# Performance work log

Measured on AMD Instinct MI355X. Metric: run time of the kernel, lower is better.

The kernel has to match this reference:

```python
import jax, jax.numpy as jnp
import numpy as np

N_NODES = 100000
N_EDGES = 1280000
IN_DIM = 64
HID = 64
OUT_DIM = 2
N_GRAPHS = 1000
BN_EPS = 1e-5


def setup_inputs() -> dict:
    key = jax.random.key(0)
    ks = jax.random.split(key, 16)
    x = jax.random.normal(ks[0], (N_NODES, IN_DIM), dtype=jnp.float32)
    edge_index = jax.random.randint(ks[1], (2, N_EDGES), 0, N_NODES, dtype=jnp.int64)
    batch = jnp.sort(jax.random.randint(ks[2], (N_NODES,), 0, N_GRAPHS, dtype=jnp.int64))
    # He-init linear weights (stored as [in, out] so forward is x @ W)
    def he(k, fan_in, fan_out):
        return jax.random.normal(k, (fan_in, fan_out), dtype=jnp.float32) * np.sqrt(2.0 / fan_in)
    return {
        "x": x,
        "edge_index": edge_index,
        "batch": batch,
        "bn_in_g": jnp.ones((IN_DIM,), jnp.float32),
        "bn_in_b": jnp.zeros((IN_DIM,), jnp.float32),
        "W1": he(ks[3], IN_DIM, HID), "b1": jnp.zeros((HID,), jnp.float32),
        "g1": jnp.ones((HID,), jnp.float32), "be1": jnp.zeros((HID,), jnp.float32),
        "W2": he(ks[4], HID, HID), "b2": jnp.zeros((HID,), jnp.float32),
        "g2": jnp.ones((HID,), jnp.float32), "be2": jnp.zeros((HID,), jnp.float32),
        "Wout": he(ks[5], HID, OUT_DIM), "bout": jnp.zeros((OUT_DIM,), jnp.float32),
    }


def _batchnorm(x, g, b):
    # training-mode BN over the node dimension (biased variance, as torch uses for normalization)
    m = jnp.mean(x, axis=0)
    v = jnp.mean(jnp.square(x - m), axis=0)
    return (x - m) * jax.lax.rsqrt(v + BN_EPS) * g + b


def _gcn_norm(edge_index, n):
    # PyG GCNConv normalization with added self-loops:
    # norm_e = deg[src]^-1/2 * deg[dst]^-1/2, deg computed on A + I over targets.
    row = jnp.concatenate([edge_index[0], jnp.arange(n, dtype=edge_index.dtype)])
    col = jnp.concatenate([edge_index[1], jnp.arange(n, dtype=edge_index.dtype)])
    deg = jax.ops.segment_sum(jnp.ones_like(col, dtype=jnp.float32), col, num_segments=n)
    dinv = jnp.where(deg > 0, jax.lax.rsqrt(deg), 0.0)
    norm = dinv[row] * dinv[col]
    return row, col, norm


def _gcn_conv(x, W, b, row, col, norm, n):
    h = x @ W                                   # [N, out]
    msg = h[row] * norm[:, None]                # gather over edges (incl. self-loops)
    agg = jax.ops.segment_sum(msg, col, num_segments=n)
    return agg + b


def reference(x, edge_index, batch, bn_in_g, bn_in_b, W1, b1, g1, be1, W2, b2, g2, be2, Wout, bout):
    n = x.shape[0]
    row, col, norm = _gcn_norm(edge_index, n)
    h = _batchnorm(x, bn_in_g, bn_in_b)         # input BN (dropout = identity in eval)
    h = _gcn_conv(h, W1, b1, row, col, norm, n)
    h = _batchnorm(jax.nn.relu(h), g1, be1)
    h = _gcn_conv(h, W2, b2, row, col, norm, n)
    h = _batchnorm(jax.nn.relu(h), g2, be2)
    # global mean pool per graph
    sums = jax.ops.segment_sum(h, batch, num_segments=N_GRAPHS)
    cnts = jax.ops.segment_sum(jnp.ones((n,), h.dtype), batch, num_segments=N_GRAPHS)
    pooled = sums / jnp.maximum(cnts, 1.0)[:, None]
    return pooled @ Wout + bout                 # [N_GRAPHS, OUT_DIM]
```

## Files before the change

### kernel.cpp

```cpp
#include <hip/hip_runtime.h>
#include <math.h>

#define N_NODES 100000
#define N_EDGES 1280000
#define DIM 64
#define N_GRAPHS 1000
#define BN_EPS 1e-5f
#define NB 392
#define P1B 256
#define P1E 5000
#define SB 400
#define WIN 64
#define NWIN (N_EDGES / WIN)
#define NSLOT 32

__device__ __forceinline__ unsigned int bf16_rtn2(float a, float b) {
    unsigned int ua = __float_as_uint(a);
    unsigned int ub = __float_as_uint(b);
    ua = (ua + 0x7FFFu + ((ua >> 16) & 1u)) >> 16;
    ub = (ub + 0x7FFFu + ((ub >> 16) & 1u)) >> 16;
    return ua | (ub << 16);
}
__device__ __forceinline__ unsigned short bf16r(float a) {
    unsigned int u = __float_as_uint(a);
    return (unsigned short)((u + 0x7FFFu + ((u >> 16) & 1u)) >> 16);
}
__device__ __forceinline__ float bfup(unsigned short u) {
    return __uint_as_float(((unsigned int)u) << 16);
}
__device__ __forceinline__ float blo(unsigned int v) { return __uint_as_float(v << 16); }
__device__ __forceinline__ float bhi(unsigned int v) { return __uint_as_float(v & 0xFFFF0000u); }

__global__ __launch_bounds__(256) void k_p1hist(const int* __restrict__ ei,
                                                const int* __restrict__ batch,
                                                const float* __restrict__ X,
                                                int* __restrict__ bh,
                                                int* __restrict__ start,
                                                float* __restrict__ gsum,
                                                float* __restrict__ gsumsq) {
    int t = threadIdx.x;
    if (blockIdx.x < P1B) {
        __shared__ int hist[NB];
        for (int b = t; b < NB; b += 256) hist[b] = 0;
        __syncthreads();
        int e0 = blockIdx.x * P1E;
        #pragma unroll 4
        for (int e = e0 + t; e < e0 + P1E; e += 256)
            atomicAdd(&hist[ei[N_EDGES + e] >> 8], 1);
        __syncthreads();
        for (int b = t; b < NB; b += 256) bh[b * P1B + blockIdx.x] = hist[b];
    } else if (blockIdx.x < P1B + SB) {
        int grp = blockIdx.x - P1B;
        int j = t & 63, rg = t >> 6;
        int base = grp * 250;
        float s = 0.f, s2 = 0.f;
        for (int i = base + rg; i < base + 250; i += 4) {
            float v = X[i * DIM + j];
            s += v; s2 += v * v;
        }
        __shared__ float ls[256], ls2[256];
        ls[t] = s; ls2[t] = s2;
        __syncthreads();
        if (t < 64) {
            int slot = (grp & (NSLOT - 1)) * DIM;
            s  = ls[j]  + ls[64 + j]  + ls[128 + j]  + ls[192 + j];
            s2 = ls2[j] + ls2[64 + j] + ls2[128 + j] + ls2[192 + j];
            atomicAdd(&gsum[slot + j], s);
            atomicAdd(&gsumsq[slot + j], s2);
        }
    } else {
        int i = (blockIdx.x - P1B - SB) * 256 + t;
        if (i < N_NODES) {
            int cur = batch[i];
            if (i == 0) { for (int q = 0; q <= cur; q++) start[q] = 0; }
            else {
                int prev = batch[i - 1];
                for (int q = prev + 1; q <= cur; q++) start[q] = i;
            }
            if (i == N_NODES - 1)
                for (int q = cur + 1; q <= N_GRAPHS; q++) start[q] = N_NODES;
        }
    }
}

__global__ void k_scan1(const int* __restrict__ bh, int* __restrict__ iscan,
                        int* __restrict__ bsum) {
    __shared__ int ls[256];
    int i = blockIdx.x * 256 + threadIdx.x;
    int v = bh[i];
    ls[threadIdx.x] = v;
    __syncthreads();
    for (int off = 1; off < 256; off <<= 1) {
        int tv = (threadIdx.x >= off) ? ls[threadIdx.x - off] : 0;
        __syncthreads();
        ls[threadIdx.x] += tv;
        __syncthreads();
    }
    iscan[i] = ls[threadIdx.x];
    if (threadIdx.x == 255) bsum[blockIdx.x] = ls[255];
}

__global__ void k_scan2(const int* __restrict__ bsum, int* __restrict__ boff) {
    __shared__ int ls[512];
    int t = threadIdx.x;
    int v0 = (t < NB) ? bsum[t] : 0;
    ls[t] = v0;
    __syncthreads();
    for (int off = 1; off < 512; off <<= 1) {
        int v = (t >= off) ? ls[t - off] : 0;
        __syncthreads();
        ls[t] += v;
        __syncthreads();
    }
    if (t < NB) boff[t] = ls[t] - v0;
}

__global__ __launch_bounds__(256) void k_p1scat(const int* __restrict__ ei,
                                                const int* __restrict__ bh,
                                                const int* __restrict__ iscan,
                                                const int* __restrict__ boff,
                                                int* __restrict__ tmp) {
    __shared__ int cur[NB];
    int blk = blockIdx.x;
    for (int b = threadIdx.x; b < NB; b += 256) {
        int i = b * P1B + blk;
        cur[b] = boff[b] + iscan[i] - bh[i];
    }
    __syncthreads();
    int e0 = blk * P1E;
    for (int e = e0 + threadIdx.x; e < e0 + P1E; e += 256) {
        int r = ei[e], c = ei[N_EDGES + e];
        int pos = atomicAdd(&cur[c >> 8], 1);
        tmp[pos] = (r << 8) | (c & 255);
    }
}

__global__ __launch_bounds__(256) void k_p2a(const int* __restrict__ tmp,
                                             const int* __restrict__ bh,
                                             const int* __restrict__ iscan,
                                             const int* __restrict__ boff,
                                             int* __restrict__ rowstart,
                                             float* __restrict__ dinv,
                                             int* __restrict__ winnode,
                                             float* __restrict__ C) {
    int b = blockIdx.x, t = threadIdx.x;
    int bstart = boff[b] + iscan[b * 256] - bh[b * 256];
    int bend = (b == NB - 1) ? N_EDGES
                             : (boff[b + 1] + iscan[(b + 1) * 256] - bh[(b + 1) * 256]);
    __shared__ int cnt[256], scn[256];
    cnt[t] = 0;
    __syncthreads();
    for (int e = bstart + t; e < bend; e += 256)
        atomicAdd(&cnt[tmp[e] & 255], 1);
    __syncthreads();
    scn[t] = cnt[t];
    __syncthreads();
    for (int off = 1; off < 256; off <<= 1) {
        int v = (t >= off) ? scn[t - off] : 0;
        __syncthreads();
        scn[t] += v;
        __syncthreads();
    }
    int node = b * 256 + t;
    int deg = cnt[t];
    int rs = bstart + scn[t] - deg;
    bool span = false;
    if (node <= N_NODES) rowstart[node] = rs;
    if (node == N_NODES) rowstart[node + 1] = rs;
    if (node < N_NODES) {
        dinv[node] = 1.0f / sqrtf((float)(deg + 1));
        int re = rs + deg;
        for (int w = (rs + WIN - 1) / WIN; w * WIN < re; ++w) winnode[w] = node;
        span = (deg > 0) && (rs / WIN != (re - 1) / WIN);
    }
    int lane = t & 63;
    int wbase = b * 256 + (t & ~63);
    unsigned long long m = __ballot(span);
    while (m) {
        int bit = __builtin_ctzll(m);
        m &= m - 1;
        C[(size_t)(wbase + bit) * DIM + lane] = 0.f;
    }
}

__global__ __launch_bounds__(256) void k_p2b(const int* __restrict__ tmp,
                                             const int* __restrict__ bh,
                                             const int* __restrict__ iscan,
                                             const int* __restrict__ boff,
                                             const int* __restrict__ rowstart,
                                             int* __restrict__ csr) {
    int b = blockIdx.x, t = threadIdx.x;
    int bstart = boff[b] + iscan[b * 256] - bh[b * 256];
    int bend = (b == NB - 1) ? N_EDGES
                             : (boff[b + 1] + iscan[(b + 1) * 256] - bh[(b + 1) * 256]);
    __shared__ int curs[256];
    int node = b * 256 + t;
    curs[t] = (node < N_NODES) ? rowstart[node] : 0;
    __syncthreads();
    for (int e = bstart + t; e < bend; e += 256) {
        int rec = tmp[e];
        int pos = atomicAdd(&curs[rec & 255], 1);
        csr[pos] = (int)((unsigned)rec >> 8);
    }
}

__global__ void k_bnfold(float* __restrict__ gsum, float* __restrict__ gsumsq,
                         const float* __restrict__ g, const float* __restrict__ b,
                         const float* __restrict__ W,
                         float* __restrict__ scale, float* __restrict__ cshift) {
    int j = threadIdx.x;
    float ms = 0.f, m2 = 0.f;
    for (int k = 0; k < NSLOT; k++) {
        ms += gsum[k * DIM + j];   gsum[k * DIM + j] = 0.f;
        m2 += gsumsq[k * DIM + j]; gsumsq[k * DIM + j] = 0.f;
    }
    float mean = ms * (1.0f / N_NODES);
    float var  = m2 * (1.0f / N_NODES) - mean * mean;
    float inv  = 1.0f / sqrtf(var + BN_EPS);
    float sc   = g[j] * inv;
    scale[j] = sc;
    __shared__ float shl[64];
    shl[j] = b[j] - mean * sc;
    __syncthreads();
    float s = 0.f;
    for (int k = 0; k < DIM; k++) s += shl[k] * W[k * DIM + j];
    cshift[j] = s;
}

__global__ void k_bnfinal(const float* __restrict__ gsum, const float* __restrict__ gsumsq,
                          const float* __restrict__ g, const float* __restrict__ b,
                          float* __restrict__ scale, float* __restrict__ shift) {
    int j = threadIdx.x;
    float ms = 0.f, m2 = 0.f;
    for (int k = 0; k < NSLOT; k++) { ms += gsum[k * DIM + j]; m2 += gsumsq[k * DIM + j]; }
    float mean = ms * (1.0f / N_NODES);
    float var  = m2 * (1.0f / N_NODES) - mean * mean;
    float inv  = 1.0f / sqrtf(var + BN_EPS);
    float sc   = g[j] * inv;
    scale[j] = sc;
    shift[j] = b[j] - mean * sc;
}

__global__ __launch_bounds__(256) void k_gemm_f32(const float* __restrict__ X,
                                                  const float* __restrict__ W,
                                                  const float* __restrict__ scale,
                                                  const float* __restrict__ cshift,
                                                  const float* __restrict__ dinv,
                                                  unsigned short* __restrict__ T) {
    __shared__ float Wl[64 * 64];
    __shared__ float Al[64 * 65];
    for (int t = threadIdx.x; t < 4096; t += 256) Wl[t] = W[t] * scale[t >> 6];
    int row0 = blockIdx.x * 64;
    for (int t = threadIdx.x; t < 4096; t += 256) {
        int r = t >> 6, k = t & 63;
        int i = row0 + r;
        Al[r * 65 + k] = (i < N_NODES) ? X[(size_t)i * DIM + k] : 0.f;
    }
    __syncthreads();
    int r = threadIdx.x & 63;
    int q = threadIdx.x >> 6;
    float acc[16];
    #pragma unroll
    for (int jj = 0; jj < 16; jj++) acc[jj] = cshift[q * 16 + jj];
    #pragma unroll 4
    for (int k = 0; k < 64; k++) {
        float a = Al[r * 65 + k];
        const float4* wv = (const float4*)&Wl[k * 64 + q * 16];
        float4 w0 = wv[0], w1 = wv[1], w2 = wv[2], w3 = wv[3];
        acc[0]  += a * w0.x; acc[1]  += a * w0.y; acc[2]  += a * w0.z; acc[3]  += a * w0.w;
        acc[4]  += a * w1.x; acc[5]  += a * w1.y; acc[6]  += a * w1.z; acc[7]  += a * w1.w;
        acc[8]  += a * w2.x; acc[9]  += a * w2.y; acc[10] += a * w2.z; acc[11] += a * w2.w;
        acc[12] += a * w3.x; acc[13] += a * w3.y; acc[14] += a * w3.z; acc[15] += a * w3.w;
    }
    int i = row0 + r;
    if (i < N_NODES) {
        float dv = dinv[i];
        unsigned int pk[8];
        #pragma unroll
        for (int jj = 0; jj < 8; jj++)
            pk[jj] = bf16_rtn2(acc[2 * jj] * dv, acc[2 * jj + 1] * dv);
        uint4* outv = (uint4*)&T[(size_t)i * DIM + q * 16];
        outv[0] = make_uint4(pk[0], pk[1], pk[2], pk[3]);
        outv[1] = make_uint4(pk[4], pk[5], pk[6], pk[7]);
    }
}

__global__ __launch_bounds__(256) void k_gemm_b16(const unsigned short* __restrict__ X,
                                                  const float* __restrict__ W,
                                                  const float* __restrict__ scale,
                                                  const float* __restrict__ cshift,
                                                  const float* __restrict__ dinv,
                                                  unsigned short* __restrict__ T) {
    __shared__ float Wl[64 * 64];
    __shared__ float Al[64 * 65];
    for (int t = threadIdx.x; t < 4096; t += 256) Wl[t] = W[t] * scale[t >> 6];
    int row0 = blockIdx.x * 64;
    for (int t = threadIdx.x; t < 4096; t += 256) {
        int r = t >> 6, k = t & 63;
        int i = row0 + r;
        Al[r * 65 + k] = (i < N_NODES) ? bfup(X[(size_t)i * DIM + k]) : 0.f;
    }
    __syncthreads();
    int r = threadIdx.x & 63;
    int q = threadIdx.x >> 6;
    float acc[16];
    #pragma unroll
    for (int jj = 0; jj < 16; jj++) acc[jj] = cshift[q * 16 + jj];
    #pragma unroll 4
    for (int k = 0; k < 64; k++) {
        float a = Al[r * 65 + k];
        const float4* wv = (const float4*)&Wl[k * 64 + q * 16];
        float4 w0 = wv[0], w1 = wv[1], w2 = wv[2], w3 = wv[3];
        acc[0]  += a * w0.x; acc[1]  += a * w0.y; acc[2]  += a * w0.z; acc[3]  += a * w0.w;
        acc[4]  += a * w1.x; acc[5]  += a * w1.y; acc[6]  += a * w1.z; acc[7]  += a * w1.w;
        acc[8]  += a * w2.x; acc[9]  += a * w2.y; acc[10] += a * w2.z; acc[11] += a * w2.w;
        acc[12] += a * w3.x; acc[13] += a * w3.y; acc[14] += a * w3.z; acc[15] += a * w3.w;
    }
    int i = row0 + r;
    if (i < N_NODES) {
        float dv = dinv[i];
        unsigned int pk[8];
        #pragma unroll
        for (int jj = 0; jj < 8; jj++)
            pk[jj] = bf16_rtn2(acc[2 * jj] * dv, acc[2 * jj + 1] * dv);
        uint4* outv = (uint4*)&T[(size_t)i * DIM + q * 16];
        outv[0] = make_uint4(pk[0], pk[1], pk[2], pk[3]);
        outv[1] = make_uint4(pk[4], pk[5], pk[6], pk[7]);
    }
}


#define SWZ(S) __builtin_amdgcn_ds_swizzle(csrv, (((S) << 5) | 0x10))

#define ISSUE(SRCV, TVV, B) do {                                      \
    SRCV[0] = SWZ(4 * (B) + 0); SRCV[1] = SWZ(4 * (B) + 1);           \
    SRCV[2] = SWZ(4 * (B) + 2); SRCV[3] = SWZ(4 * (B) + 3);           \
    TVV[0] = T2[(unsigned)SRCV[0] * 16u + cc];                        \
    TVV[1] = T2[(unsigned)SRCV[1] * 16u + cc];                        \
    TVV[2] = T2[(unsigned)SRCV[2] * 16u + cc];                        \
    TVV[3] = T2[(unsigned)SRCV[3] * 16u + cc];                        \
} while (0)

#define STEP(TVV, U, B, FL) do {                                      \
    const int ebs = e0 + 16 * (B) + 4 * (U);                          \
    uint2 tvv = TVV[U];                                               \
    float a0 = blo(tvv.x), a1 = bhi(tvv.x);                           \
    float a2 = blo(tvv.y), a3 = bhi(tvv.y);                           \
    if (re > ebs + 3) {                                               \
        acc0 += a0; acc1 += a1; acc2 += a2; acc3 += a3;               \
    } else {                                                          \
        int lo = ebs;                                                 \
        while (re <= ebs + 3) {                                       \
            int eg = ebs + gg;                                        \
            if (eg >= lo && eg < re) {                                \
                acc0 += a0; acc1 += a1; acc2 += a2; acc3 += a3;       \
            }                                                         \
            lo = re;                                                  \
            FL();                                                     \
        }                                                             \
        if (ebs + gg >= lo) {                                         \
            acc0 += a0; acc1 += a1; acc2 += a2; acc3 += a3;           \
        }                                                             \
    }                                                                 \
} while (0)

#define CONSUME(TVV, B, FL) do {                                      \
    STEP(TVV, 0, B, FL); STEP(TVV, 1, B, FL);                         \
    STEP(TVV, 2, B, FL); STEP(TVV, 3, B, FL);                         \
} while (0)

#define COMB4()                                                       \
    float t0 = acc0 + __shfl_xor(acc0, 16); t0 += __shfl_xor(t0, 32); \
    float t1 = acc1 + __shfl_xor(acc1, 16); t1 += __shfl_xor(t1, 32); \
    float t2 = acc2 + __shfl_xor(acc2, 16); t2 += __shfl_xor(t2, 32); \
    float t3 = acc3 + __shfl_xor(acc3, 16); t3 += __shfl_xor(t3, 32);

#define ADVANCE() do {                                                \
    acc0 = acc1 = acc2 = acc3 = 0.f;                                  \
    ++i; ++k;                                                         \
    if (k < 64) re = __builtin_amdgcn_readlane(rsv, k);               \
    else        re = __builtin_amdgcn_readfirstlane(rowstart[i + 1]); \
    tsv = T2[(unsigned)i * 16u + cc];                                 \
} while (0)

#define FLUSH1() do {                                                 \
    COMB4();                                                          \
    if (part) {                                                       \
        if (lane < 16) {                                              \
            float* cp = &C[(size_t)i * DIM + 4 * cc];                 \
            atomicAdd(cp + 0, t0); atomicAdd(cp + 1, t1);             \
            atomicAdd(cp + 2, t2); atomicAdd(cp + 3, t3);             \
        }                                                             \
        part = false;                                                 \
    } else {                                                          \
        int cnt = i - i0;                                             \
        float di;                                                     \
        if (cnt < 64)                                                 \
            di = __int_as_float(                                      \
                __builtin_amdgcn_readlane(__float_as_int(dv), cnt));  \
        else di = dinv[i];                                            \
        float h0 = fmaxf((t0 + blo(tsv.x)) * di + bb.x, 0.f);         \
        float h1 = fmaxf((t1 + bhi(tsv.x)) * di + bb.y, 0.f);         \
        float h2 = fmaxf((t2 + blo(tsv.y)) * di + bb.z, 0.f);         \
        float h3 = fmaxf((t3 + bhi(tsv.y)) * di + bb.w, 0.f);         \
        if (lane < 16)                                                \
            ((uint2*)H)[(unsigned)i * 16u + cc] =                     \
                make_uint2(bf16_rtn2(h0, h1), bf16_rtn2(h2, h3));     \
        s0 += h0; s1 += h1; s2 += h2; s3 += h3;                       \
        q0 += h0 * h0; q1 += h1 * h1; q2 += h2 * h2; q3 += h3 * h3;   \
    }                                                                 \
    ADVANCE();                                                        \
} while (0)

__global__ __launch_bounds__(256) void k_gather1(const unsigned short* __restrict__ T,
                                                 const float* __restrict__ dinv,
                                                 const int* __restrict__ rowstart,
                                                 const int* __restrict__ winnode,
                                                 const int* __restrict__ csr,
                                                 const float* __restrict__ bias,
                                                 float* __restrict__ C,
                                                 unsigned short* __restrict__ H,
                                                 float* __restrict__ gsum,
                                                 float* __restrict__ gsumsq) {
    const int lane = threadIdx.x & 63;
    const int gg = lane >> 4;
    const int cc = lane & 15;
    const int w = blockIdx.x * 4 + (threadIdx.x >> 6);
    const int e0 = w * WIN;
    const int eend = e0 + WIN;
    const uint2* T2 = (const uint2*)T;

    int csrv = csr[e0 + 4 * cc + gg];
    int i0 = __builtin_amdgcn_readfirstlane(winnode[w]);
    int rsv = rowstart[min(i0 + lane, N_NODES + 1)];
    float dv = dinv[min(i0 + lane, N_NODES - 1)];
    uint2 tsv = T2[(unsigned)i0 * 16u + cc];
    const float4 bb = ((const float4*)bias)[cc];

    int i = i0, k = 1;
    int re = __builtin_amdgcn_readlane(rsv, 1);
    bool part = __builtin_amdgcn_readlane(rsv, 0) < e0;
    float acc0 = 0.f, acc1 = 0.f, acc2 = 0.f, acc3 = 0.f;
    float s0 = 0.f, s1 = 0.f, s2 = 0.f, s3 = 0.f;
    float q0 = 0.f, q1 = 0.f, q2 = 0.f, q3 = 0.f;

    int srcA[4], srcB[4], srcC[4], srcD[4];
    uint2 tva[4], tvb[4], tvc[4], tvd[4];
    ISSUE(srcA, tva, 0);
    ISSUE(srcB, tvb, 1);
    ISSUE(srcC, tvc, 2);
    ISSUE(srcD, tvd, 3);
    CONSUME(tva, 0, FLUSH1);
    CONSUME(tvb, 1, FLUSH1);
    CONSUME(tvc, 2, FLUSH1);
    CONSUME(tvd, 3, FLUSH1);

    if (part || re > eend) {
        COMB4();
        if (lane < 16) {
            float* cp = &C[(size_t)i * DIM + 4 * cc];
            atomicAdd(cp + 0, t0); atomicAdd(cp + 1, t1);
            atomicAdd(cp + 2, t2); atomicAdd(cp + 3, t3);
        }
    } else {
        FLUSH1();
    }

    __shared__ float shs[4][64], shq[4][64];
    int wv = threadIdx.x >> 6;
    if (lane < 16) {
        shs[wv][4 * cc + 0] = s0; shs[wv][4 * cc + 1] = s1;
        shs[wv][4 * cc + 2] = s2; shs[wv][4 * cc + 3] = s3;
        shq[wv][4 * cc + 0] = q0; shq[wv][4 * cc + 1] = q1;
        shq[wv][4 * cc + 2] = q2; shq[wv][4 * cc + 3] = q3;
    }
    __syncthreads();
    if (threadIdx.x < 64) {
        int j = threadIdx.x;
        float vs = shs[0][j] + shs[1][j] + shs[2][j] + shs[3][j];
        float vq = shq[0][j] + shq[1][j] + shq[2][j] + shq[3][j];
        int slot = (blockIdx.x & (NSLOT - 1)) * DIM;
        atomicAdd(&gsum[slot + j], vs);
        atomicAdd(&gsumsq[slot + j], vq);
    }
}

#define FLUSH2() do {                                                 \
    COMB4();                                                          \
    if (part) {                                                       \
        if (lane < 16) {                                              \
            float* cp = &C[(size_t)i * DIM + 4 * cc];                 \
            atomicAdd(cp + 0, t0); atomicAdd(cp + 1, t1);             \
            atomicAdd(cp + 2, t2); atomicAdd(cp + 3, t3);             \
        }                                                             \
        part = false;                                                 \
    } else {                                                          \
        int cnt = i - i0;                                             \
        float di;                                                     \
        int gi;                                                       \
        if (cnt < 64) {                                               \
            di = __int_as_float(                                      \
                __builtin_amdgcn_readlane(__float_as_int(dv), cnt));  \
            gi = __builtin_amdgcn_readlane(bv, cnt);                  \
        } else { di = dinv[i]; gi = batch[i]; }                       \
        float h0 = fmaxf((t0 + blo(tsv.x)) * di + bb.x, 0.f);         \
        float h1 = fmaxf((t1 + bhi(tsv.x)) * di + bb.y, 0.f);         \
        float h2 = fmaxf((t2 + blo(tsv.y)) * di + bb.z, 0.f);         \
        float h3 = fmaxf((t3 + bhi(tsv.y)) * di + bb.w, 0.f);         \
        s0 += h0; s1 += h1; s2 += h2; s3 += h3;                       \
        q0 += h0 * h0; q1 += h1 * h1; q2 += h2 * h2; q3 += h3 * h3;   \
        if (gi != cur_g) {                                            \
            if (cur_g >= 0 && lane < 16) {                            \
                float* pp = &pool[(size_t)cur_g * DIM + 4 * cc];      \
                atomicAdd(pp + 0, ps0); atomicAdd(pp + 1, ps1);       \
                atomicAdd(pp + 2, ps2); atomicAdd(pp + 3, ps3);       \
            }                                                         \
            ps0 = ps1 = ps2 = ps3 = 0.f;                              \
            cur_g = gi;                                               \
        }                                                             \
        ps0 += h0; ps1 += h1; ps2 += h2; ps3 += h3;                   \
    }                                                                 \
    ADVANCE();                                                        \
} while (0)

__global__ __launch_bounds__(256) void k_gather2(const unsigned short* __restrict__ T,
                                                 const float* __restrict__ dinv,
                                                 const int* __restrict__ rowstart,
                                                 const int* __restrict__ winnode,
                                                 const int* __restrict__ csr,
                                                 const float* __restrict__ bias,
                                                 const int* __restrict__ batch,
                                                 float* __restrict__ C,
                                                 float* __restrict__ pool,
                                                 float* __restrict__ gsum,
                                                 float* __restrict__ gsumsq) {
    const int lane = threadIdx.x & 63;
    const int gg = lane >> 4;
    const int cc = lane & 15;
    const int w = blockIdx.x * 4 + (threadIdx.x >> 6);
    const int e0 = w * WIN;
    const int eend = e0 + WIN;
    const uint2* T2 = (const uint2*)T;

    int csrv = csr[e0 + 4 * cc + gg];
    int i0 = __builtin_amdgcn_readfirstlane(winnode[w]);
    int rsv = rowstart[min(i0 + lane, N_NODES + 1)];
    float dv = dinv[min(i0 + lane, N_NODES - 1)];
    int bv = batch[min(i0 + lane, N_NODES - 1)];
    uint2 tsv = T2[(unsigned)i0 * 16u + cc];
    const float4 bb = ((const float4*)bias)[cc];

    int i = i0, k = 1;
    int re = __builtin_amdgcn_readlane(rsv, 1);
    bool part = __builtin_amdgcn_readlane(rsv, 0) < e0;
    float acc0 = 0.f, acc1 = 0.f, acc2 = 0.f, acc3 = 0.f;
    float s0 = 0.f, s1 = 0.f, s2 = 0.f, s3 = 0.f;
    float q0 = 0.f, q1 = 0.f, q2 = 0.f, q3 = 0.f;
    float ps0 = 0.f, ps1 = 0.f, ps2 = 0.f, ps3 = 0.f;
    int cur_g = -1;

    int srcA[4], srcB[4], srcC[4], srcD[4];
    uint2 tva[4], tvb[4], tvc[4], tvd[4];
    ISSUE(srcA, tva, 0);
    ISSUE(srcB, tvb, 1);
    ISSUE(srcC, tvc, 2);
    ISSUE(srcD, tvd, 3);
    CONSUME(tva, 0, FLUSH2);
    CONSUME(tvb, 1, FLUSH2);
    CONSUME(tvc, 2, FLUSH2);
    CONSUME(tvd, 3, FLUSH2);

    if (part || re > eend) {
        COMB4();
        if (lane < 16) {
            float* cp = &C[(size_t)i * DIM + 4 * cc];
            atomicAdd(cp + 0, t0); atomicAdd(cp + 1, t1);
            atomicAdd(cp + 2, t2); atomicAdd(cp + 3, t3);
        }
    } else {
        FLUSH2();
    }
    if (cur_g >= 0 && lane < 16) {
        float* pp = &pool[(size_t)cur_g * DIM + 4 * cc];
        atomicAdd(pp + 0, ps0); atomicAdd(pp + 1, ps1);
        atomicAdd(pp + 2, ps2); atomicAdd(pp + 3, ps3);
    }

    __shared__ float shs[4][64], shq[4][64];
    int wv = threadIdx.x >> 6;
    if (lane < 16) {
        shs[wv][4 * cc + 0] = s0; shs[wv][4 * cc + 1] = s1;
        shs[wv][4 * cc + 2] = s2; shs[wv][4 * cc + 3] = s3;
        shq[wv][4 * cc + 0] = q0; shq[wv][4 * cc + 1] = q1;
        shq[wv][4 * cc + 2] = q2; shq[wv][4 * cc + 3] = q3;
    }
    __syncthreads();
    if (threadIdx.x < 64) {
        int j = threadIdx.x;
        float vs = shs[0][j] + shs[1][j] + shs[2][j] + shs[3][j];
        float vq = shq[0][j] + shq[1][j] + shq[2][j] + shq[3][j];
        int slot = (blockIdx.x & (NSLOT - 1)) * DIM;
        atomicAdd(&gsum[slot + j], vs);
        atomicAdd(&gsumsq[slot + j], vq);
    }
}

__global__ __launch_bounds__(256) void k_strad1(float* __restrict__ C,
                                                const unsigned short* __restrict__ T,
                                                const float* __restrict__ dinv,
                                                const int* __restrict__ rowstart,
                                                const int* __restrict__ winnode,
                                                const float* __restrict__ bias,
                                                unsigned short* __restrict__ H,
                                                float* __restrict__ gsum,
                                                float* __restrict__ gsumsq) {
    int lane = threadIdx.x & 63;
    int wv = threadIdx.x >> 6;
    float bb = bias[lane];
    float s = 0.f, s2 = 0.f;
    __shared__ int anyw;
    if (threadIdx.x == 0) anyw = 0;
    __syncthreads();
    if (blockIdx.x < NWIN / 4) {
        int w = blockIdx.x * 4 + wv;
        int n = winnode[w];
        int rs = rowstart[n];
        if (w == rs / WIN + 1) {
            float di = dinv[n];
            float c = C[(size_t)n * DIM + lane];
            C[(size_t)n * DIM + lane] = 0.f;
            float h = fmaxf((c + bfup(T[(size_t)n * DIM + lane])) * di + bb, 0.f);
            H[(size_t)n * DIM + lane] = bf16r(h);
            s += h; s2 += h * h;
            anyw = 1;
        }
    } else {
        int base = (blockIdx.x - NWIN / 4) * 256 + wv * 64;
        int nb = base + lane;
        int d0 = 0;
        if (nb < N_NODES)
            d0 = (rowstart[nb + 1] == rowstart[nb]) && ((rowstart[nb] & (WIN - 1)) == 0);
        unsigned long long m = __ballot(d0);
        while (m) {
            int b = __builtin_ctzll(m);
            m &= m - 1;
            int n = base + b;
            float di = dinv[n];
            float h = fmaxf(bfup(T[(size_t)n * DIM + lane]) * di + bb, 0.f);
            H[(size_t)n * DIM + lane] = bf16r(h);
            s += h; s2 += h * h;
            anyw = 1;
        }
    }
    __shared__ float ls[256], ls2[256];
    ls[threadIdx.x] = s; ls2[threadIdx.x] = s2;
    __syncthreads();
    if (anyw && threadIdx.x < 64) {
        int j = threadIdx.x;
        int slot = (blockIdx.x & (NSLOT - 1)) * DIM;
        atomicAdd(&gsum[slot + j],   ls[j] + ls[64 + j] + ls[128 + j] + ls[192 + j]);
        atomicAdd(&gsumsq[slot + j], ls2[j] + ls2[64 + j] + ls2[128 + j] + ls2[192 + j]);
    }
}

__global__ __launch_bounds__(256) void k_strad2(const float* __restrict__ C,
                                                const unsigned short* __restrict__ T,
                                                const float* __restrict__ dinv,
                                                const int* __restrict__ rowstart,
                                                const int* __restrict__ winnode,
                                                const float* __restrict__ bias,
                                                const int* __restrict__ batch,
                                                float* __restrict__ pool,
                                                float* __restrict__ gsum,
                                                float* __restrict__ gsumsq) {
    int lane = threadIdx.x & 63;
    int wv = threadIdx.x >> 6;
    float bb = bias[lane];
    float s = 0.f, s2 = 0.f;
    __shared__ int anyw;
    if (threadIdx.x == 0) anyw = 0;
    __syncthreads();
    if (blockIdx.x < NWIN / 4) {
        int w = blockIdx.x * 4 + wv;
        int n = winnode[w];
        int rs = rowstart[n];
        if (w == rs / WIN + 1) {
            float di = dinv[n];
            float h = fmaxf((C[(size_t)n * DIM + lane]
                             + bfup(T[(size_t)n * DIM + lane])) * di + bb, 0.f);
            s += h; s2 += h * h;
            atomicAdd(&pool[(size_t)batch[n] * DIM + lane], h);
            anyw = 1;
        }
    } else {
        int base = (blockIdx.x - NWIN / 4) * 256 + wv * 64;
        int nb = base + lane;
        int d0 = 0;
        if (nb < N_NODES)
            d0 = (rowstart[nb + 1] == rowstart[nb]) && ((rowstart[nb] & (WIN - 1)) == 0);
        unsigned long long m = __ballot(d0);
        while (m) {
            int b = __builtin_ctzll(m);
            m &= m - 1;
            int n = base + b;
            float di = dinv[n];
            float h = fmaxf(bfup(T[(size_t)n * DIM + lane]) * di + bb, 0.f);
            s += h; s2 += h * h;
            atomicAdd(&pool[(size_t)batch[n] * DIM + lane], h);
            anyw = 1;
        }
    }
    __shared__ float ls[256], ls2[256];
    ls[threadIdx.x] = s; ls2[threadIdx.x] = s2;
    __syncthreads();
    if (anyw && threadIdx.x < 64) {
        int j = threadIdx.x;
        int slot = (blockIdx.x & (NSLOT - 1)) * DIM;
        atomicAdd(&gsum[slot + j],   ls[j] + ls[64 + j] + ls[128 + j] + ls[192 + j]);
        atomicAdd(&gsumsq[slot + j], ls2[j] + ls2[64 + j] + ls2[128 + j] + ls2[192 + j]);
    }
}

__global__ void k_final(const float* __restrict__ pool, const int* __restrict__ start,
                        const float* __restrict__ scale, const float* __restrict__ shift,
                        const float* __restrict__ Wout, const float* __restrict__ bout,
                        float* __restrict__ out) {
    int g = blockIdx.x;
    int l = threadIdx.x;
    float c = fmaxf((float)(start[g + 1] - start[g]), 1.f);
    float p = (pool[g * DIM + l] / c) * scale[l] + shift[l];
    float a0 = p * Wout[l * 2 + 0];
    float a1 = p * Wout[l * 2 + 1];
    #pragma unroll
    for (int off = 32; off; off >>= 1) {
        a0 += __shfl_down(a0, off, 64);
        a1 += __shfl_down(a1, off, 64);
    }
    if (l == 0) {
        out[g * 2 + 0] = a0 + bout[0];
        out[g * 2 + 1] = a1 + bout[1];
    }
}

extern "C" void kernel_launch(void* const* d_in, const int* in_sizes, int n_in,
                              void* d_out, int out_size, void* d_ws, size_t ws_size,
                              hipStream_t stream) {
    (void)in_sizes; (void)n_in; (void)out_size; (void)ws_size;
    const float* x       = (const float*)d_in[0];
    const int*   ei      = (const int*)d_in[1];
    const int*   batch   = (const int*)d_in[2];
    const float* bn_in_g = (const float*)d_in[3];
    const float* bn_in_b = (const float*)d_in[4];
    const float* W1      = (const float*)d_in[5];
    const float* b1      = (const float*)d_in[6];
    const float* g1      = (const float*)d_in[7];
    const float* be1     = (const float*)d_in[8];
    const float* W2      = (const float*)d_in[9];
    const float* b2      = (const float*)d_in[10];
    const float* g2      = (const float*)d_in[11];
    const float* be2     = (const float*)d_in[12];
    const float* Wout    = (const float*)d_in[13];
    const float* bout    = (const float*)d_in[14];
    float* out = (float*)d_out;

    char* p = (char*)d_ws;
    float* C = (float*)p;                   p += (size_t)N_NODES * DIM * 4;
    unsigned short* H = (unsigned short*)p; p += (size_t)N_NODES * DIM * 2;
    unsigned short* T = (unsigned short*)p; p += (size_t)N_NODES * DIM * 2;
    int* csr = (int*)p;                     p += (size_t)N_EDGES * 4;
    float* dinv = (float*)p;                p += N_NODES * 4;
    int* bh = (int*)p;                      p += NB * P1B * 4;
    int* iscan = (int*)p;                   p += NB * P1B * 4;
    int* rowstart = (int*)p;                p += (N_NODES + 2) * 4;
    int* winnode = (int*)p;                 p += NWIN * 4;
    int* bsum = (int*)p;                    p += NB * 4;
    int* boff = (int*)p;                    p += NB * 4;
    int* start = (int*)p;                   p += (N_GRAPHS + 2) * 4;
    float* gsum = (float*)p;                p += NSLOT * DIM * 4;
    float* gsumsq = (float*)p;              p += NSLOT * DIM * 4;
    float* scale = (float*)p;               p += DIM * 4;
    float* shift = (float*)p;               p += DIM * 4;
    float* cshift = (float*)p;              p += DIM * 4;
    float* pool = (float*)p;                p += (size_t)N_GRAPHS * DIM * 4;
    int* tmp = (int*)H;

    hipMemsetAsync(gsum, 0, 2 * NSLOT * DIM * sizeof(float), stream);
    hipMemsetAsync(pool, 0, (size_t)N_GRAPHS * DIM * sizeof(float), stream);
    k_p1hist<<<P1B + SB + 392, 256, 0, stream>>>(ei, batch, x, bh, start, gsum, gsumsq);
    k_scan1<<<NB, 256, 0, stream>>>(bh, iscan, bsum);
    k_scan2<<<1, 512, 0, stream>>>(bsum, boff);
    k_p1scat<<<P1B, 256, 0, stream>>>(ei, bh, iscan, boff, tmp);
    k_p2a<<<NB, 256, 0, stream>>>(tmp, bh, iscan, boff, rowstart, dinv, winnode, C);
    k_p2b<<<NB, 256, 0, stream>>>(tmp, bh, iscan, boff, rowstart, csr);

    k_bnfold<<<1, 64, 0, stream>>>(gsum, gsumsq, bn_in_g, bn_in_b, W1, scale, cshift);
    k_gemm_f32<<<(N_NODES + 63) / 64, 256, 0, stream>>>(x, W1, scale, cshift, dinv, T);
    k_gather1<<<NWIN / 4, 256, 0, stream>>>(T, dinv, rowstart, winnode, csr, b1,
                                            C, H, gsum, gsumsq);
    k_strad1<<<NWIN / 4 + 392, 256, 0, stream>>>(C, T, dinv, rowstart, winnode, b1,
                                                 H, gsum, gsumsq);

    k_bnfold<<<1, 64, 0, stream>>>(gsum, gsumsq, g1, be1, W2, scale, cshift);
    k_gemm_b16<<<(N_NODES + 63) / 64, 256, 0, stream>>>(H, W2, scale, cshift, dinv, T);
    k_gather2<<<NWIN / 4, 256, 0, stream>>>(T, dinv, rowstart, winnode, csr, b2,
                                            batch, C, pool, gsum, gsumsq);
    k_strad2<<<NWIN / 4 + 392, 256, 0, stream>>>(C, T, dinv, rowstart, winnode, b2,
                                                 batch, pool, gsum, gsumsq);

    k_bnfinal<<<1, 64, 0, stream>>>(gsum, gsumsq, g2, be2, scale, shift);
    k_final<<<N_GRAPHS, 64, 0, stream>>>(pool, start, scale, shift, Wout, bout, out);
}
```

Measured before the change: 374.2 us.

## Double gather window to 128 edges with overlapped reissue and lane-spread atomics

Each wavefront now handles 128 edges instead of 64, loading two CSR chunks and issuing the second chunk's gathers right after each first-chunk group is consumed, which keeps loads in flight. This halves the number of waves and the per-window overhead (rowstart/dinv/batch loads, partial-row atomics, BN stat atomics). Partial-row and pool atomics are also redistributed so all 64 lanes each do one atomic instead of 16 lanes doing four. Risks include more live registers reducing occupancy and fewer waves lowering load balance.

```diff
diff --git a/kernel.cpp b/kernel.cpp
--- a/kernel.cpp
+++ b/kernel.cpp
@@ -10,7 +10,7 @@
 #define P1B 256
 #define P1E 5000
 #define SB 400
-#define WIN 64
+#define WIN 128
 #define NWIN (N_EDGES / WIN)
 #define NSLOT 32
 
@@ -330,11 +330,11 @@
 }
 
 
-#define SWZ(S) __builtin_amdgcn_ds_swizzle(csrv, (((S) << 5) | 0x10))
-
-#define ISSUE(SRCV, TVV, B) do {                                      \
-    SRCV[0] = SWZ(4 * (B) + 0); SRCV[1] = SWZ(4 * (B) + 1);           \
-    SRCV[2] = SWZ(4 * (B) + 2); SRCV[3] = SWZ(4 * (B) + 3);           \
+#define SWZ(V, S) __builtin_amdgcn_ds_swizzle((V), (((S) << 5) | 0x10))
+
+#define ISSUE(SRCV, TVV, CV, S0) do {                                 \
+    SRCV[0] = SWZ(CV, (S0) + 0); SRCV[1] = SWZ(CV, (S0) + 1);         \
+    SRCV[2] = SWZ(CV, (S0) + 2); SRCV[3] = SWZ(CV, (S0) + 3);         \
     TVV[0] = T2[(unsigned)SRCV[0] * 16u + cc];                        \
     TVV[1] = T2[(unsigned)SRCV[1] * 16u + cc];                        \
     TVV[2] = T2[(unsigned)SRCV[2] * 16u + cc];                        \
@@ -375,6 +375,14 @@
     float t2 = acc2 + __shfl_xor(acc2, 16); t2 += __shfl_xor(t2, 32); \
     float t3 = acc3 + __shfl_xor(acc3, 16); t3 += __shfl_xor(t3, 32);
 
+#define REDIST64(OUT, V0, V1, V2, V3)                                 \
+    float _r0 = __shfl((V0), lane >> 2);                              \
+    float _r1 = __shfl((V1), lane >> 2);                              \
+    float _r2 = __shfl((V2), lane >> 2);                              \
+    float _r3 = __shfl((V3), lane >> 2);                              \
+    float OUT = (lane & 2) ? ((lane & 1) ? _r3 : _r2)                 \
+                           : ((lane & 1) ? _r1 : _r0);
+
 #define ADVANCE() do {                                                \
     acc0 = acc1 = acc2 = acc3 = 0.f;                                  \
     ++i; ++k;                                                         \
@@ -386,11 +394,8 @@
 #define FLUSH1() do {                                                 \
     COMB4();                                                          \
     if (part) {                                                       \
-        if (lane < 16) {                                              \
-            float* cp = &C[(size_t)i * DIM + 4 * cc];                 \
-            atomicAdd(cp + 0, t0); atomicAdd(cp + 1, t1);             \
-            atomicAdd(cp + 2, t2); atomicAdd(cp + 3, t3);             \
-        }                                                             \
+        REDIST64(cv, t0, t1, t2, t3);                                 \
+        atomicAdd(&C[(size_t)i * DIM + lane], cv);                    \
         part = false;                                                 \
     } else {                                                          \
         int cnt = i - i0;                                             \
@@ -430,7 +435,8 @@
     const int eend = e0 + WIN;
     const uint2* T2 = (const uint2*)T;
 
-    int csrv = csr[e0 + 4 * cc + gg];
+    int csrv0 = csr[e0 + 4 * cc + gg];
+    int csrv1 = csr[e0 + 64 + 4 * cc + gg];
     int i0 = __builtin_amdgcn_readfirstlane(winnode[w]);
     int rsv = rowstart[min(i0 + lane, N_NODES + 1)];
     float dv = dinv[min(i0 + lane, N_NODES - 1)];
@@ -446,22 +452,23 @@
 
     int srcA[4], srcB[4], srcC[4], srcD[4];
     uint2 tva[4], tvb[4], tvc[4], tvd[4];
-    ISSUE(srcA, tva, 0);
-    ISSUE(srcB, tvb, 1);
-    ISSUE(srcC, tvc, 2);
-    ISSUE(srcD, tvd, 3);
-    CONSUME(tva, 0, FLUSH1);
-    CONSUME(tvb, 1, FLUSH1);
-    CONSUME(tvc, 2, FLUSH1);
-    CONSUME(tvd, 3, FLUSH1);
+    ISSUE(srcA, tva, csrv0, 0);
+    ISSUE(srcB, tvb, csrv0, 4);
+    ISSUE(srcC, tvc, csrv0, 8);
+    ISSUE(srcD, tvd, csrv0, 12);
+    CONSUME(tva, 0, FLUSH1);  ISSUE(srcA, tva, csrv1, 0);
+    CONSUME(tvb, 1, FLUSH1);  ISSUE(srcB, tvb, csrv1, 4);
+    CONSUME(tvc, 2, FLUSH1);  ISSUE(srcC, tvc, csrv1, 8);
+    CONSUME(tvd, 3, FLUSH1);  ISSUE(srcD, tvd, csrv1, 12);
+    CONSUME(tva, 4, FLUSH1);
+    CONSUME(tvb, 5, FLUSH1);
+    CONSUME(tvc, 6, FLUSH1);
+    CONSUME(tvd, 7, FLUSH1);
 
     if (part || re > eend) {
         COMB4();
-        if (lane < 16) {
-            float* cp = &C[(size_t)i * DIM + 4 * cc];
-            atomicAdd(cp + 0, t0); atomicAdd(cp + 1, t1);
-            atomicAdd(cp + 2, t2); atomicAdd(cp + 3, t3);
-        }
+        REDIST64(cv, t0, t1, t2, t3);
+        atomicAdd(&C[(size_t)i * DIM + lane], cv);
     } else {
         FLUSH1();
     }
@@ -488,11 +495,8 @@
 #define FLUSH2() do {                                                 \
     COMB4();                                                          \
     if (part) {                                                       \
-        if (lane < 16) {                                              \
-            float* cp = &C[(size_t)i * DIM + 4 * cc];                 \
-            atomicAdd(cp + 0, t0); atomicAdd(cp + 1, t1);             \
-            atomicAdd(cp + 2, t2); atomicAdd(cp + 3, t3);             \
-        }                                                             \
+        REDIST64(cv, t0, t1, t2, t3);                                 \
+        atomicAdd(&C[(size_t)i * DIM + lane], cv);                    \
         part = false;                                                 \
     } else {                                                          \
         int cnt = i - i0;                                             \
@@ -510,10 +514,9 @@
         s0 += h0; s1 += h1; s2 += h2; s3 += h3;                       \
         q0 += h0 * h0; q1 += h1 * h1; q2 += h2 * h2; q3 += h3 * h3;   \
         if (gi != cur_g) {                                            \
-            if (cur_g >= 0 && lane < 16) {                            \
-                float* pp = &pool[(size_t)cur_g * DIM + 4 * cc];      \
-                atomicAdd(pp + 0, ps0); atomicAdd(pp + 1, ps1);       \
-                atomicAdd(pp + 2, ps2); atomicAdd(pp + 3, ps3);       \
+            if (cur_g >= 0) {                                         \
+                REDIST64(pv, ps0, ps1, ps2, ps3);                     \
+                atomicAdd(&pool[(size_t)cur_g * DIM + lane], pv);     \
             }                                                         \
             ps0 = ps1 = ps2 = ps3 = 0.f;                              \
             cur_g = gi;                                               \
@@ -542,7 +545,8 @@
     const int eend = e0 + WIN;
     const uint2* T2 = (const uint2*)T;
 
-    int csrv = csr[e0 + 4 * cc + gg];
+    int csrv0 = csr[e0 + 4 * cc + gg];
+    int csrv1 = csr[e0 + 64 + 4 * cc + gg];
     int i0 = __builtin_amdgcn_readfirstlane(winnode[w]);
     int rsv = rowstart[min(i0 + lane, N_NODES + 1)];
     float dv = dinv[min(i0 + lane, N_NODES - 1)];
@@ -561,29 +565,29 @@
 
     int srcA[4], srcB[4], srcC[4], srcD[4];
     uint2 tva[4], tvb[4], tvc[4], tvd[4];
-    ISSUE(srcA, tva, 0);
-    ISSUE(srcB, tvb, 1);
-    ISSUE(srcC, tvc, 2);
-    ISSUE(srcD, tvd, 3);
-    CONSUME(tva, 0, FLUSH2);
-    CONSUME(tvb, 1, FLUSH2);
-    CONSUME(tvc, 2, FLUSH2);
-    CONSUME(tvd, 3, FLUSH2);
+    ISSUE(srcA, tva, csrv0, 0);
+    ISSUE(srcB, tvb, csrv0, 4);
+    ISSUE(srcC, tvc, csrv0, 8);
+    ISSUE(srcD, tvd, csrv0, 12);
+    CONSUME(tva, 0, FLUSH2);  ISSUE(srcA, tva, csrv1, 0);
+    CONSUME(tvb, 1, FLUSH2);  ISSUE(srcB, tvb, csrv1, 4);
+    CONSUME(tvc, 2, FLUSH2);  ISSUE(srcC, tvc, csrv1, 8);
+    CONSUME(tvd, 3, FLUSH2);  ISSUE(srcD, tvd, csrv1, 12);
+    CONSUME(tva, 4, FLUSH2);
+    CONSUME(tvb, 5, FLUSH2);
+    CONSUME(tvc, 6, FLUSH2);
+    CONSUME(tvd, 7, FLUSH2);
 
     if (part || re > eend) {
         COMB4();
-        if (lane < 16) {
-            float* cp = &C[(size_t)i * DIM + 4 * cc];
-            atomicAdd(cp + 0, t0); atomicAdd(cp + 1, t1);
-            atomicAdd(cp + 2, t2); atomicAdd(cp + 3, t3);
-        }
+        REDIST64(cv, t0, t1, t2, t3);
+        atomicAdd(&C[(size_t)i * DIM + lane], cv);
     } else {
         FLUSH2();
     }
-    if (cur_g >= 0 && lane < 16) {
-        float* pp = &pool[(size_t)cur_g * DIM + 4 * cc];
-        atomicAdd(pp + 0, ps0); atomicAdd(pp + 1, ps1);
-        atomicAdd(pp + 2, ps2); atomicAdd(pp + 3, ps3);
+    if (cur_g >= 0) {
+        REDIST64(pv, ps0, ps1, ps2, ps3);
+        atomicAdd(&pool[(size_t)cur_g * DIM + lane], pv);
     }
 
     __shared__ float shs[4][64], shq[4][64];
```

Result: faster. 317.3 us (-15.2%).
